# Performance work log

Hardware: AMD Instinct MI355X
Metric: run time of the kernel (lower is better)

Reference implementation:

```python
import jax, jax.numpy as jnp
import numpy as np

E = 1024
H = 16
DH = E // H
EPS = 1e-09


def setup_inputs() -> dict:
    key = jax.random.key(0)
    ks = jax.random.split(key, 12)
    B, S = 2, 2048
    scale = 1.0 / np.sqrt(E)
    inp = {
        "query": jax.random.normal(ks[0], (B, S, E), dtype=jnp.float32),
        "key": jax.random.normal(ks[1], (B, S, E), dtype=jnp.float32),
        "value": jax.random.normal(ks[2], (B, S, E), dtype=jnp.float32),
        "mask": jax.random.randint(ks[3], (B, 1, S, S), 0, 2, dtype=jnp.int32),
        "Wq": jax.random.normal(ks[4], (E, E), dtype=jnp.float32) * scale,
        "bq": jnp.zeros((E,), dtype=jnp.float32),
        "Wk": jax.random.normal(ks[5], (E, E), dtype=jnp.float32) * scale,
        "bk": jnp.zeros((E,), dtype=jnp.float32),
        "Wv": jax.random.normal(ks[6], (E, E), dtype=jnp.float32) * scale,
        "bv": jnp.zeros((E,), dtype=jnp.float32),
        "Wo": jax.random.normal(ks[7], (E, E), dtype=jnp.float32) * scale,
        "bo": jnp.zeros((E,), dtype=jnp.float32),
    }
    return inp


def _split_heads(x):
    # [B,S,E] -> [B,H,S,DH]
    B, S, _ = x.shape
    return x.reshape(B, S, H, DH).transpose(0, 2, 1, 3)


def reference(query, key, value, mask, Wq, bq, Wk, bk, Wv, bv, Wo, bo):
    q = _split_heads(query @ Wq.T + bq)
    k = _split_heads(key @ Wk.T + bk)
    v = _split_heads(value @ Wv.T + bv)
    # scores: [B,H,Sq,Sk]; NOTE: original module applies NO softmax.
    scores = jnp.einsum("bhqd,bhkd->bhqk", q, k) / np.sqrt(DH)
    # masked_fill_(mask == 0, epsilon): replace masked positions with 1e-9
    scores = jnp.where(mask == 0, jnp.float32(EPS), scores)
    # dropout p=0.0 (eval) -> identity
    out = jnp.einsum("bhqk,bhkd->bhqd", scores, v)
    B, _, S, _ = out.shape
    out = out.transpose(0, 2, 1, 3).reshape(B, S, E)
    return out @ Wo.T + bo
```

## Files before the change

kernel.cpp:

```cpp
#include <hip/hip_runtime.h>
#include <hip/hip_bf16.h>
#include <stdint.h>
#include <stddef.h>

#define SB 2
#define SS 2048
#define SE 1024
#define SH 16
#define SD 64

typedef __attribute__((ext_vector_type(8))) short bf16x8;
typedef __attribute__((ext_vector_type(4))) float f32x4;

__device__ __forceinline__ short f2bf(float f) {
    union { float f; uint32_t u; } v; v.f = f;
    uint32_t u = v.u;
    uint32_t r = (u + 0x7fffu + ((u >> 16) & 1u)) >> 16;
    return (short)(uint16_t)r;
}

__device__ __forceinline__ uint32_t pkmask(float a, float b, uint32_t bits) {
    union { float f; uint32_t u; } ua, ub;
    ua.f = a; ub.f = b;
    uint32_t ra = (bits & 1u) ? (ua.u + 0x7fffu + ((ua.u >> 16) & 1u)) : 0u;
    uint32_t rb = (bits & 2u) ? (ub.u + 0x7fffu + ((ub.u >> 16) & 1u)) : 0u;
    return (rb & 0xffff0000u) | (ra >> 16);
}

__device__ __forceinline__ void gld16(const short* g, short* l) {
    __builtin_amdgcn_global_load_lds(
        (const __attribute__((address_space(1))) unsigned int*)g,
        (__attribute__((address_space(3))) unsigned int*)l, 16, 0, 0);
}

struct CvtArgs {
    const float* src[7];
    short* dst[7];
    int nblk[7];
};

__global__ __launch_bounds__(256) void cvt_bf16(CvtArgs a) {
    const int j = blockIdx.y;
    if (blockIdx.x >= a.nblk[j]) return;
    const size_t i = ((size_t)blockIdx.x * 256 + threadIdx.x) * 8;
    const float* s = a.src[j] + i;
    f32x4 f0 = *(const f32x4*)s;
    f32x4 f1 = *(const f32x4*)(s + 4);
    bf16x8 o;
    o[0] = f2bf(f0[0]); o[1] = f2bf(f0[1]); o[2] = f2bf(f0[2]); o[3] = f2bf(f0[3]);
    o[4] = f2bf(f1[0]); o[5] = f2bf(f1[1]); o[6] = f2bf(f1[2]); o[7] = f2bf(f1[3]);
    *(bf16x8*)(a.dst[j] + i) = o;
}

__global__ __launch_bounds__(256) void pack_mask(const int* __restrict__ m,
                                                 unsigned long long* __restrict__ mp) {
    const int lane = threadIdx.x & 63;
    int wv = (blockIdx.x * 256 + threadIdx.x) >> 6;
    const int NW = SB * SS * (SS / 64);
    const int stride = (gridDim.x * 256) >> 6;
    for (int wd = wv; wd < NW; wd += stride) {
        int v = m[(size_t)wd * 64 + lane];
        unsigned long long bb = __ballot(v != 0);
        if (lane == 0) {
            int b = wd >> 16;
            int q = (wd >> 5) & 2047;
            int kw = wd & 31;
            mp[((size_t)b << 16) + kw * 2048 + q] = bb;
        }
    }
}

struct GemmJob {
    const short* A; const short* W; const float* bias; void* C;
    int mode;
    float scale;
};

template <bool OUTF32>
__global__ __launch_bounds__(256, 3) void gemm128(GemmJob j0, GemmJob j1, GemmJob j2) {
    GemmJob j = (blockIdx.z == 0) ? j0 : (blockIdx.z == 1) ? j1 : j2;
    __shared__ short As[128 * 64];
    __shared__ short Bs[128 * 64];

    const int m0 = blockIdx.y * 128;
    const int n0 = blockIdx.x * 128;
    const int tid = threadIdx.x;
    const int lane = tid & 63;
    const int w = tid >> 6;
    const int wm = (w >> 1) * 64;
    const int wn = (w & 1) * 64;
    const int quad = lane >> 4;
    const int l16 = lane & 15;

    f32x4 acc[4][4] = {};

    for (int k0 = 0; k0 < 1024; k0 += 64) {
#pragma unroll
        for (int i = 0; i < 4; ++i) {
            int ch = lane + 64 * (w * 4 + i);
            int row = ch >> 3;
            int col = (ch & 7) * 8;
            gld16(j.A + (size_t)(m0 + row) * 1024 + k0 + col, &As[(w * 4 + i) * 512]);
            gld16(j.W + (size_t)(n0 + row) * 1024 + k0 + col, &Bs[(w * 4 + i) * 512]);
        }
        __syncthreads();
#pragma unroll
        for (int ks = 0; ks < 2; ++ks) {
            bf16x8 af[4], bfr[4];
#pragma unroll
            for (int mi = 0; mi < 4; ++mi)
                af[mi] = *(const bf16x8*)&As[(wm + mi * 16 + l16) * 64 + ks * 32 + quad * 8];
#pragma unroll
            for (int ni = 0; ni < 4; ++ni)
                bfr[ni] = *(const bf16x8*)&Bs[(wn + ni * 16 + l16) * 64 + ks * 32 + quad * 8];
#pragma unroll
            for (int mi = 0; mi < 4; ++mi)
#pragma unroll
                for (int ni = 0; ni < 4; ++ni)
                    acc[mi][ni] = __builtin_amdgcn_mfma_f32_16x16x32_bf16(
                        af[mi], bfr[ni], acc[mi][ni], 0, 0, 0);
        }
        __syncthreads();
    }

#pragma unroll
    for (int mi = 0; mi < 4; ++mi) {
#pragma unroll
        for (int ni = 0; ni < 4; ++ni) {
            int n = n0 + wn + ni * 16 + l16;
            float bv = j.bias[n];
#pragma unroll
            for (int r = 0; r < 4; ++r) {
                int m = m0 + wm + mi * 16 + quad * 4 + r;
                float v = (acc[mi][ni][r] + bv) * j.scale;
                if (OUTF32) {
                    ((float*)j.C)[(size_t)m * 1024 + n] = v;
                } else {
                    short o = f2bf(v);
                    short* C = (short*)j.C;
                    if (j.mode == 0) {
                        C[(size_t)m * 1024 + n] = o;
                    } else {
                        int b = m >> 11, s = m & 2047;
                        int hh = n >> 6, d = n & 63;
                        if (j.mode == 1)
                            C[(((size_t)(b * SH + hh) * SS) + s) * SD + d] = o;
                        else
                            C[(((size_t)(b * SH + hh) * SD) + d) * SS + s] = o;
                    }
                }
            }
        }
    }
}

__global__ __launch_bounds__(256, 2) void attn2(
    const short* __restrict__ Q,
    const short* __restrict__ Kk,
    const short* __restrict__ Vt,
    const unsigned long long* __restrict__ MpT,
    short* __restrict__ O) {
    __shared__ __align__(16) short Ks[2][64 * 72];
    __shared__ __align__(16) short Vs[2][64 * 72];

    const int qt = blockIdx.x;
    const int bh = blockIdx.y;
    const int b = bh >> 4;
    const int h = bh & 15;

    const short* qbase = Q + (size_t)bh * SS * SD;
    const short* kbase = Kk + (size_t)bh * SS * SD;
    const short* vbase = Vt + (size_t)bh * SD * SS;
    const unsigned long long* mTb = MpT + ((size_t)b << 16);

    const int tid = threadIdx.x;
    const int lane = tid & 63;
    const int w = tid >> 6;
    const int quad = lane >> 4;
    const int l16 = lane & 15;
    const int qw = qt * 128 + w * 32;

    bf16x8 qf[2][2];
#pragma unroll
    for (int u = 0; u < 2; ++u) {
        qf[u][0] = *(const bf16x8*)(qbase + (size_t)(qw + u * 16 + l16) * SD + quad * 8);
        qf[u][1] = *(const bf16x8*)(qbase + (size_t)(qw + u * 16 + l16) * SD + 32 + quad * 8);
    }

    f32x4 oacc[2][4] = {};

    bf16x8 kpf[2], vpf[2];
    int prow[2], pcol[2];
#pragma unroll
    for (int r = 0; r < 2; ++r) {
        int ch = tid + r * 256;
        prow[r] = ch >> 3;
        pcol[r] = (ch & 7) * 8;
    }
    auto loadKV = [&](int k0) {
#pragma unroll
        for (int r = 0; r < 2; ++r) {
            kpf[r] = *(const bf16x8*)(kbase + (size_t)(k0 + prow[r]) * SD + pcol[r]);
            vpf[r] = *(const bf16x8*)(vbase + (size_t)prow[r] * SS + k0 + pcol[r]);
        }
    };
    auto storeKV = [&](int buf) {
#pragma unroll
        for (int r = 0; r < 2; ++r) {
            *(bf16x8*)&Ks[buf][prow[r] * 72 + pcol[r]] = kpf[r];
            *(bf16x8*)&Vs[buf][prow[r] * 72 + pcol[r]] = vpf[r];
        }
    };

    loadKV(0);
    int cur = 0;

    for (int k0 = 0; k0 < SS; k0 += 64) {
        storeKV(cur);
        if (k0 + 64 < SS) loadKV(k0 + 64);
        unsigned long long wq0 = mTb[(k0 >> 6) * 2048 + qw + l16];
        unsigned long long wq1 = mTb[(k0 >> 6) * 2048 + qw + 16 + l16];
        __syncthreads();

        const short* KsB = &Ks[cur][0];
        const short* VsB = &Vs[cur][0];
#pragma unroll
        for (int p = 0; p < 2; ++p) {
            const int s0 = p * 2, s1 = p * 2 + 1;
            bf16x8 a00 = *(const bf16x8*)&KsB[(s0 * 16 + l16) * 72 + quad * 8];
            bf16x8 a01 = *(const bf16x8*)&KsB[(s0 * 16 + l16) * 72 + 32 + quad * 8];
            bf16x8 a10 = *(const bf16x8*)&KsB[(s1 * 16 + l16) * 72 + quad * 8];
            bf16x8 a11 = *(const bf16x8*)&KsB[(s1 * 16 + l16) * 72 + 32 + quad * 8];

            union SCU { uint32_t d[4]; bf16x8 v; } scf[2];
#pragma unroll
            for (int u = 0; u < 2; ++u) {
                f32x4 sA = {}, sB = {};
                sA = __builtin_amdgcn_mfma_f32_16x16x32_bf16(a00, qf[u][0], sA, 0, 0, 0);
                sA = __builtin_amdgcn_mfma_f32_16x16x32_bf16(a01, qf[u][1], sA, 0, 0, 0);
                sB = __builtin_amdgcn_mfma_f32_16x16x32_bf16(a10, qf[u][0], sB, 0, 0, 0);
                sB = __builtin_amdgcn_mfma_f32_16x16x32_bf16(a11, qf[u][1], sB, 0, 0, 0);

                unsigned long long w64 = u ? wq1 : wq0;
                uint32_t sh0 = (uint32_t)(w64 >> (s0 * 16 + quad * 4));
                uint32_t sh1 = (uint32_t)(w64 >> (s1 * 16 + quad * 4));
                scf[u].d[0] = pkmask(sA[0], sA[1], sh0);
                scf[u].d[1] = pkmask(sA[2], sA[3], sh0 >> 2);
                scf[u].d[2] = pkmask(sB[0], sB[1], sh1);
                scf[u].d[3] = pkmask(sB[2], sB[3], sh1 >> 2);
            }

#pragma unroll
            for (int di = 0; di < 4; ++di) {
                union { uint32_t d[4]; bf16x8 v; } vb;
                const uint32_t* vlo =
                    (const uint32_t*)&VsB[(di * 16 + l16) * 72 + s0 * 16 + quad * 4];
                const uint32_t* vhi =
                    (const uint32_t*)&VsB[(di * 16 + l16) * 72 + s1 * 16 + quad * 4];
                vb.d[0] = vlo[0]; vb.d[1] = vlo[1];
                vb.d[2] = vhi[0]; vb.d[3] = vhi[1];
                oacc[0][di] = __builtin_amdgcn_mfma_f32_16x16x32_bf16(
                    scf[0].v, vb.v, oacc[0][di], 0, 0, 0);
                oacc[1][di] = __builtin_amdgcn_mfma_f32_16x16x32_bf16(
                    scf[1].v, vb.v, oacc[1][di], 0, 0, 0);
            }
        }
        cur ^= 1;
    }

#pragma unroll
    for (int u = 0; u < 2; ++u) {
#pragma unroll
        for (int di = 0; di < 4; ++di) {
            int d = di * 16 + l16;
#pragma unroll
            for (int r = 0; r < 4; ++r) {
                int qg2 = qw + u * 16 + quad * 4 + r;
                O[((size_t)b * SS + qg2) * SE + h * SD + d] = f2bf(oacc[u][di][r]);
            }
        }
    }
}

extern "C" void kernel_launch(void* const* d_in, const int* in_sizes, int n_in,
                              void* d_out, int out_size, void* d_ws,
                              size_t ws_size, hipStream_t stream) {
    const float* query = (const float*)d_in[0];
    const float* key   = (const float*)d_in[1];
    const float* value = (const float*)d_in[2];
    const int*   mask  = (const int*)d_in[3];
    float* out = (float*)d_out;

    const size_t NEL = (size_t)SB * SS * SE;
    unsigned long long* Mp = (unsigned long long*)d_out;
    short* mb   = (short*)d_in[3];
    short* qbf  = mb;
    short* kbf  = mb + NEL;
    short* vbf  = mb + 2 * NEL;
    short* Wqb  = mb + 3 * NEL;
    short* Wkb  = Wqb + SE * SE;
    short* Wvb  = Wkb + SE * SE;
    short* Wob  = Wvb + SE * SE;
    short* Qb   = (short*)d_in[0];
    short* Om   = (short*)d_in[0] + NEL;
    short* Kb   = (short*)d_in[1];
    short* Vtb  = (short*)d_in[2];

    dim3 tblk(256);

    pack_mask<<<dim3(1024), tblk, 0, stream>>>(mask, Mp);

    CvtArgs ca;
    ca.src[0] = query; ca.dst[0] = qbf; ca.nblk[0] = 2048;
    ca.src[1] = key;   ca.dst[1] = kbf; ca.nblk[1] = 2048;
    ca.src[2] = value; ca.dst[2] = vbf; ca.nblk[2] = 2048;
    ca.src[3] = (const float*)d_in[4];  ca.dst[3] = Wqb; ca.nblk[3] = 512;
    ca.src[4] = (const float*)d_in[6];  ca.dst[4] = Wkb; ca.nblk[4] = 512;
    ca.src[5] = (const float*)d_in[8];  ca.dst[5] = Wvb; ca.nblk[5] = 512;
    ca.src[6] = (const float*)d_in[10]; ca.dst[6] = Wob; ca.nblk[6] = 512;
    cvt_bf16<<<dim3(2048, 7), tblk, 0, stream>>>(ca);

    GemmJob jq{qbf, Wqb, (const float*)d_in[5], Qb,  1, 0.125f};
    GemmJob jv{vbf, Wvb, (const float*)d_in[9], Vtb, 2, 1.0f};
    GemmJob jk{kbf, Wkb, (const float*)d_in[7], Kb,  1, 1.0f};
    gemm128<false><<<dim3(8, 32, 3), tblk, 0, stream>>>(jq, jv, jk);

    attn2<<<dim3(SS / 128, SB * SH), tblk, 0, stream>>>(Qb, Kb, Vtb, Mp, Om);

    gemm128<true><<<dim3(8, 32, 1), tblk, 0, stream>>>(
        GemmJob{Om, Wob, (const float*)d_in[11], out, 0, 1.0f},
        GemmJob{Om, Wob, (const float*)d_in[11], out, 0, 1.0f},
        GemmJob{Om, Wob, (const float*)d_in[11], out, 0, 1.0f});
}
```

Before: 279.0 us.

## Split attention over key dimension into two partial passes and sum

Splits the attention kernel's key loop into two halves via a third grid dimension, each writing a bf16 partial output buffer, then adds a small kernel to sum the partials into the final attention output. This doubles the block count from 512 to 1024 for better CU occupancy and raises the launch-bounds occupancy hint from 2 to 4. It costs an extra kernel launch, extra global traffic for the two partial buffers, and an extra bf16 rounding step on the partial sums.

```diff
diff --git a/kernel.cpp b/kernel.cpp
--- a/kernel.cpp
+++ b/kernel.cpp
@@ -17,6 +17,12 @@
     uint32_t u = v.u;
     uint32_t r = (u + 0x7fffu + ((u >> 16) & 1u)) >> 16;
     return (short)(uint16_t)r;
+}
+
+__device__ __forceinline__ float bf2f(short s) {
+    union { uint32_t u; float f; } v;
+    v.u = (uint32_t)(uint16_t)s << 16;
+    return v.f;
 }
 
 __device__ __forceinline__ uint32_t pkmask(float a, float b, uint32_t bits) {
@@ -68,6 +74,18 @@
             mp[((size_t)b << 16) + kw * 2048 + q] = bb;
         }
     }
+}
+
+__global__ __launch_bounds__(256) void add_po(const short* __restrict__ p0,
+                                              const short* __restrict__ p1,
+                                              short* __restrict__ o) {
+    const size_t i = ((size_t)blockIdx.x * 256 + threadIdx.x) * 8;
+    bf16x8 a = *(const bf16x8*)(p0 + i);
+    bf16x8 b = *(const bf16x8*)(p1 + i);
+    bf16x8 r;
+#pragma unroll
+    for (int j = 0; j < 8; ++j) r[j] = f2bf(bf2f(a[j]) + bf2f(b[j]));
+    *(bf16x8*)(o + i) = r;
 }
 
 struct GemmJob {
@@ -154,12 +172,13 @@
     }
 }
 
-__global__ __launch_bounds__(256, 2) void attn2(
+__global__ __launch_bounds__(256, 4) void attn2(
     const short* __restrict__ Q,
     const short* __restrict__ Kk,
     const short* __restrict__ Vt,
     const unsigned long long* __restrict__ MpT,
-    short* __restrict__ O) {
+    short* __restrict__ P0,
+    short* __restrict__ P1) {
     __shared__ __align__(16) short Ks[2][64 * 72];
     __shared__ __align__(16) short Vs[2][64 * 72];
 
@@ -167,6 +186,8 @@
     const int bh = blockIdx.y;
     const int b = bh >> 4;
     const int h = bh & 15;
+    const int kbeg = blockIdx.z << 10;
+    short* po = blockIdx.z ? P1 : P0;
 
     const short* qbase = Q + (size_t)bh * SS * SD;
     const short* kbase = Kk + (size_t)bh * SS * SD;
@@ -212,12 +233,12 @@
         }
     };
 
-    loadKV(0);
+    loadKV(kbeg);
     int cur = 0;
 
-    for (int k0 = 0; k0 < SS; k0 += 64) {
+    for (int k0 = kbeg; k0 < kbeg + 1024; k0 += 64) {
         storeKV(cur);
-        if (k0 + 64 < SS) loadKV(k0 + 64);
+        if (k0 + 64 < kbeg + 1024) loadKV(k0 + 64);
         unsigned long long wq0 = mTb[(k0 >> 6) * 2048 + qw + l16];
         unsigned long long wq1 = mTb[(k0 >> 6) * 2048 + qw + 16 + l16];
         __syncthreads();
@@ -276,7 +297,7 @@
 #pragma unroll
             for (int r = 0; r < 4; ++r) {
                 int qg2 = qw + u * 16 + quad * 4 + r;
-                O[((size_t)b * SS + qg2) * SE + h * SD + d] = f2bf(oacc[u][di][r]);
+                po[((size_t)b * SS + qg2) * SE + h * SD + d] = f2bf(oacc[u][di][r]);
             }
         }
     }
@@ -302,9 +323,11 @@
     short* Wvb  = Wkb + SE * SE;
     short* Wob  = Wvb + SE * SE;
     short* Qb   = (short*)d_in[0];
-    short* Om   = (short*)d_in[0] + NEL;
+    short* P0   = Qb + NEL;
     short* Kb   = (short*)d_in[1];
+    short* P1   = Kb + NEL;
     short* Vtb  = (short*)d_in[2];
+    short* Om   = Vtb + NEL;
 
     dim3 tblk(256);
 
@@ -325,7 +348,9 @@
     GemmJob jk{kbf, Wkb, (const float*)d_in[7], Kb,  1, 1.0f};
     gemm128<false><<<dim3(8, 32, 3), tblk, 0, stream>>>(jq, jv, jk);
 
-    attn2<<<dim3(SS / 128, SB * SH), tblk, 0, stream>>>(Qb, Kb, Vtb, Mp, Om);
+    attn2<<<dim3(SS / 128, SB * SH, 2), tblk, 0, stream>>>(Qb, Kb, Vtb, Mp, P0, P1);
+
+    add_po<<<dim3(2048), tblk, 0, stream>>>(P0, P1, Om);
 
     gemm128<true><<<dim3(8, 32, 1), tblk, 0, stream>>>(
         GemmJob{Om, Wob, (const float*)d_in[11], out, 0, 1.0f},
```

Measured after the change: 275.7 us. No clear change (-1.2%).
